# Optimization experiments

Measured on AMD Instinct MI355X. Metric: run time of the kernel, lower is better.

## Reference

```python
import jax, jax.numpy as jnp
import numpy as np
from jax import lax

N = 51200            # total nodes
E = 409600           # edges
FEAT = 768           # BERT emb size
HID = 256            # GGNN out_channels
L = 6                # GGNN layers
NPG = 200            # nodes per graph (conv1d_1 in_channels)
C1_OUT, K1, P1 = 50, 3, 1
C2_OUT, K2 = 20, 1
MP1_K, MP1_S = 3, 2
MP2_K, MP2_S = 2, 2

def _pooled_len(n):
    n = (n - MP1_K) // MP1_S + 1
    n = (n - MP2_K) // MP2_S + 1
    return n

def setup_inputs():
    key = jax.random.key(0)
    ks = jax.random.split(key, 12)
    s = lambda i, shape: jax.random.normal(ks[i], shape, jnp.float32) * 0.02
    fc1_in = C2_OUT * _pooled_len(HID + FEAT)  # 20*255 = 5100
    fc2_in = C2_OUT * _pooled_len(HID)         # 20*63  = 1260
    return dict(
        x=jax.random.normal(ks[0], (N, FEAT), jnp.float32),
        edge_index=jax.random.randint(ks[1], (2, E), 0, N, dtype=jnp.int32),
        W_in=s(2, (HID, FEAT)), b_in=jnp.zeros((HID,), jnp.float32),
        W_ggnn=s(3, (L, HID, HID)),
        W_ih=s(4, (3 * HID, HID)), W_hh=s(5, (3 * HID, HID)),
        b_ih=jnp.zeros((3 * HID,), jnp.float32), b_hh=jnp.zeros((3 * HID,), jnp.float32),
        Wc1=s(6, (C1_OUT, NPG, K1)), bc1=jnp.zeros((C1_OUT,), jnp.float32),
        Wc2=s(7, (C2_OUT, C1_OUT, K2)), bc2=jnp.zeros((C2_OUT,), jnp.float32),
        Wf1=s(8, (1, fc1_in)), bf1=jnp.zeros((1,), jnp.float32),
        Wf2=s(9, (1, fc2_in)), bf2=jnp.zeros((1,), jnp.float32),
    )

def _conv1d(x, w, b, pad):
    y = lax.conv_general_dilated(x, w, (1,), [(pad, pad)], dimension_numbers=('NCH', 'OIH', 'NCH'))
    return y + b[None, :, None]

def _maxpool1d(x, k, s):
    return lax.reduce_window(x, -jnp.inf, lax.max, (1, 1, k), (1, 1, s), 'VALID')

def _ggnn(h0, src, dst, W_ggnn, W_ih, W_hh, b_ih, b_hh):
    h = h0
    for i in range(L):  # fixed small layer loop
        m = h @ W_ggnn[i]                                   # [N, HID]
        agg = jax.ops.segment_sum(m[src], dst, num_segments=N)  # scatter-add aggr
        gi = agg @ W_ih.T + b_ih                            # GRUCell input gates
        gh = h @ W_hh.T + b_hh                              # GRUCell hidden gates
        i_r, i_z, i_n = jnp.split(gi, 3, axis=1)
        h_r, h_z, h_n = jnp.split(gh, 3, axis=1)
        r = jax.nn.sigmoid(i_r + h_r)
        z = jax.nn.sigmoid(i_z + h_z)
        n = jnp.tanh(i_n + r * h_n)
        h = (1.0 - z) * n + z * h
    return h

def _conv_head(h, x, Wc1, bc1, Wc2, bc2, Wf1, bf1, Wf2, bf2):
    concat = jnp.concatenate([h, x], axis=1).reshape(-1, NPG, HID + FEAT)  # [G, NPG, 1024]
    Z = _maxpool1d(jax.nn.relu(_conv1d(concat, Wc1, bc1, P1)), MP1_K, MP1_S)
    Z = _maxpool1d(_conv1d(Z, Wc2, bc2, 0), MP2_K, MP2_S)
    Y = h.reshape(-1, NPG, HID)
    Y = _maxpool1d(jax.nn.relu(_conv1d(Y, Wc1, bc1, P1)), MP1_K, MP1_S)
    Y = _maxpool1d(_conv1d(Y, Wc2, bc2, 0), MP2_K, MP2_S)
    z = Z.reshape(Z.shape[0], -1) @ Wf1.T + bf1
    y = Y.reshape(Y.shape[0], -1) @ Wf2.T + bf2
    # dropout p=0.2 is identity in eval mode
    return jax.nn.sigmoid((z * y).ravel())  # [G]

def reference(x, edge_index, W_in, b_in, W_ggnn, W_ih, W_hh, b_ih, b_hh, Wc1, bc1, Wc2, bc2, Wf1, bf1, Wf2, bf2):
    h0 = x @ W_in.T + b_in
    h = _ggnn(h0, edge_index[0], edge_index[1], W_ggnn, W_ih, W_hh, b_ih, b_hh)
    p = _conv_head(h, x, Wc1, bc1, Wc2, bc2, Wf1, bf1, Wf2, bf2)
    eps = 1e-6
    p = jnp.clip(p, eps, 1.0 - eps)
    z1 = jnp.log(p / (1.0 - p))
    return jnp.stack([jnp.zeros_like(z1), z1], axis=1)  # [G, 2]
```

## Files before the change

kernel.cpp:

```cpp
#include <hip/hip_runtime.h>
#include <math.h>

#define N_NODES 51200
#define N_EDGES 409600
#define FEAT    768
#define HID     256
#define NPG     200
#define G_GRAPHS 256

typedef _Float16 f16x8 __attribute__((ext_vector_type(8)));
typedef _Float16 f16x4 __attribute__((ext_vector_type(4)));
typedef float    f32x4 __attribute__((ext_vector_type(4)));

__device__ __forceinline__ void cvt4(const float* __restrict__ in, _Float16* __restrict__ out, int i) {
    float4 v = *(const float4*)&in[i * 4];
    f16x4 h;
    h[0] = (_Float16)v.x; h[1] = (_Float16)v.y; h[2] = (_Float16)v.z; h[3] = (_Float16)v.w;
    *(f16x4*)&out[i * 4] = h;
}

__global__ __launch_bounds__(256) void k_prep(const float* __restrict__ W_in, const float* __restrict__ W_ih,
                                              const float* __restrict__ W_hh, const float* __restrict__ W_g,
                                              const float* __restrict__ x, const float* __restrict__ Wc1,
                                              const float* __restrict__ bih, const float* __restrict__ bhh,
                                              _Float16* __restrict__ Win_h, _Float16* __restrict__ Wih_h,
                                              _Float16* __restrict__ Whh_h, _Float16* __restrict__ Wg_h,
                                              _Float16* __restrict__ XF, _Float16* __restrict__ Wp,
                                              float* __restrict__ brz, float* __restrict__ bnn,
                                              _Float16* __restrict__ Wrz2,
                                              int* __restrict__ deg, int* __restrict__ fill) {
    int id = blockIdx.x * 256 + threadIdx.x;
    if (id < 49152) { cvt4(W_in, Win_h, id); return; }
    id -= 49152;
    if (id < 49152) { cvt4(W_ih, Wih_h, id); return; }
    id -= 49152;
    if (id < 49152) { cvt4(W_hh, Whh_h, id); return; }
    id -= 49152;
    if (id < 98304) { cvt4(W_g, Wg_h, id); return; }
    id -= 98304;
    if (id < 49152) {
        int ch = id / 12288, r = id - ch * 12288;
        int o = r / 192, k = r - o * 192;
        int dk = k >> 6, cc = k & 63;
        int c = ch * 64 + cc;
        float v = 0.f;
        if (o < 50 && c < NPG) v = Wc1[(o * NPG + c) * 3 + dk];
        Wp[id] = (_Float16)v;
        return;
    }
    id -= 49152;
    if (id < 1024) {
        if (id < 512) brz[id] = bih[id] + bhh[id];
        else {
            int q = id - 512;
            bnn[q] = (q < 256) ? bih[512 + q] : bhh[512 + (q - 256)];
        }
        return;
    }
    id -= 1024;
    if (id < 786432) {
        int l = id >> 17, r = id & 131071;
        int j = r >> 8, c = r & 255;
        Wrz2[(size_t)l * 262144 + j * 512 + 256 + c] = (_Float16)W_hh[j * 256 + c];
        return;
    }
    id -= 786432;
    if (id < 12800) { *(int4*)&deg[id * 4] = make_int4(0, 0, 0, 0); return; }
    id -= 12800;
    if (id < 12800) { *(int4*)&fill[id * 4] = make_int4(0, 0, 0, 0); return; }
    id -= 12800;
    if (id < 9830400) { cvt4(x, XF, id); return; }
}

__global__ __launch_bounds__(256) void k_deg(const int* __restrict__ ei, int* __restrict__ deg) {
    int e = blockIdx.x * 256 + threadIdx.x;
    if (e < N_EDGES) atomicAdd(&deg[ei[N_EDGES + e]], 1);
}

__global__ __launch_bounds__(1024) void k_scan(const int* __restrict__ deg, int* __restrict__ rowp) {
    __shared__ int sums[1024];
    int tid = threadIdx.x;
    int base = tid * 50;
    int s = 0;
    for (int j = 0; j < 50; ++j) s += deg[base + j];
    sums[tid] = s;
    __syncthreads();
    for (int off = 1; off < 1024; off <<= 1) {
        int v = 0;
        if (tid >= off) v = sums[tid - off];
        __syncthreads();
        sums[tid] += v;
        __syncthreads();
    }
    int run = sums[tid] - s;
    for (int j = 0; j < 50; ++j) { rowp[base + j] = run; run += deg[base + j]; }
    if (tid == 1023) rowp[N_NODES] = run;
}

__global__ __launch_bounds__(256) void k_fill(const int* __restrict__ ei, const int* __restrict__ rowp,
                                              int* __restrict__ fill, int* __restrict__ col) {
    int e = blockIdx.x * 256 + threadIdx.x;
    if (e < N_EDGES) {
        int d = ei[N_EDGES + e];
        int pos = atomicAdd(&fill[d], 1);
        col[rowp[d] + pos] = ei[e];
    }
}

template<int AF16, int OUT, int COLB, int SWZ>
__global__ __launch_bounds__(256) void k_gemm2(const void* __restrict__ Av, int lda,
                                               const _Float16* __restrict__ B,
                                               const float* __restrict__ bias,
                                               void* __restrict__ Cv, int ldc,
                                               int K, int wgPerL, int aLStride, int bLStride,
                                               int cLStride, int biasStride) {
    __shared__ _Float16 As[128 * 64];
    __shared__ _Float16 Bs[128 * 64];
    int wg = blockIdx.x;
    int l = wg / wgPerL; wg -= l * wgPerL;
    if (AF16) Av = (const void*)((const _Float16*)Av + (size_t)l * aLStride);
    else      Av = (const void*)((const float*)Av + (size_t)l * aLStride);
    B += (size_t)l * bLStride;
    if (bias) bias += (size_t)l * biasStride;
    if (OUT == 1) Cv = (void*)((_Float16*)Cv + (size_t)l * cLStride);
    else          Cv = (void*)((float*)Cv + (size_t)l * cLStride);
    int rowBase, colBase;
    if (SWZ) {
        int xcd = wg & 7, t = wg >> 3;
        int cb = t % COLB, gidx = t / COLB;
        rowBase = (gidx * 8 + xcd) * 128;
        colBase = cb * 128;
    } else {
        rowBase = (wg / COLB) * 128;
        colBase = (wg % COLB) * 128;
    }
    int tid = threadIdx.x;
    int lane = tid & 63;
    int wid = tid >> 6;
    int wr = wid >> 1, wc = wid & 1;
    f32x4 acc[4][4] = {};
    for (int k0 = 0; k0 < K; k0 += 64) {
        __syncthreads();
        #pragma unroll
        for (int p = 0; p < 4; ++p) {
            int c = p * 256 + tid;
            int row = c >> 3, slot = c & 7;
            int dst = row * 64 + ((slot ^ (row & 7)) * 8);
            if (AF16) {
                const _Float16* srcA = (const _Float16*)Av + (size_t)(rowBase + row) * lda + k0 + slot * 8;
                *(f16x8*)&As[dst] = *(const f16x8*)srcA;
            } else {
                const float* srcA = (const float*)Av + (size_t)(rowBase + row) * lda + k0 + slot * 8;
                float4 f0 = *(const float4*)srcA;
                float4 f1 = *(const float4*)(srcA + 4);
                f16x8 hv;
                hv[0] = (_Float16)f0.x; hv[1] = (_Float16)f0.y; hv[2] = (_Float16)f0.z; hv[3] = (_Float16)f0.w;
                hv[4] = (_Float16)f1.x; hv[5] = (_Float16)f1.y; hv[6] = (_Float16)f1.z; hv[7] = (_Float16)f1.w;
                *(f16x8*)&As[dst] = hv;
            }
            const _Float16* srcB = B + (size_t)(colBase + row) * K + k0 + slot * 8;
            *(f16x8*)&Bs[dst] = *(const f16x8*)srcB;
        }
        __syncthreads();
        #pragma unroll
        for (int ks = 0; ks < 2; ++ks) {
            f16x8 af[4], bf[4];
            #pragma unroll
            for (int mi = 0; mi < 4; ++mi) {
                int row = wr * 64 + mi * 16 + (lane & 15);
                int slot = (lane >> 4) + ks * 4;
                af[mi] = *(const f16x8*)&As[row * 64 + ((slot ^ (row & 7)) * 8)];
            }
            #pragma unroll
            for (int nj = 0; nj < 4; ++nj) {
                int row = wc * 64 + nj * 16 + (lane & 15);
                int slot = (lane >> 4) + ks * 4;
                bf[nj] = *(const f16x8*)&Bs[row * 64 + ((slot ^ (row & 7)) * 8)];
            }
            #pragma unroll
            for (int mi = 0; mi < 4; ++mi)
                #pragma unroll
                for (int nj = 0; nj < 4; ++nj)
                    acc[mi][nj] = __builtin_amdgcn_mfma_f32_16x16x32_f16(af[mi], bf[nj], acc[mi][nj], 0, 0, 0);
        }
    }
    #pragma unroll
    for (int mi = 0; mi < 4; ++mi) {
        #pragma unroll
        for (int nj = 0; nj < 4; ++nj) {
            int col = colBase + wc * 64 + nj * 16 + (lane & 15);
            float bv = bias ? bias[col] : 0.f;
            #pragma unroll
            for (int r = 0; r < 4; ++r) {
                int row = rowBase + wr * 64 + mi * 16 + (lane >> 4) * 4 + r;
                float val = acc[mi][nj][r] + bv;
                if (OUT == 0) ((float*)Cv)[(size_t)row * ldc + col] = val;
                else          ((_Float16*)Cv)[(size_t)row * ldc + col] = (_Float16)val;
            }
        }
    }
}

__global__ __launch_bounds__(256) void k_gemmrz(const _Float16* __restrict__ S, const _Float16* __restrict__ hc,
                                                const _Float16* __restrict__ B, const float* __restrict__ bias,
                                                _Float16* __restrict__ C) {
    __shared__ _Float16 As[128 * 64];
    __shared__ _Float16 Bs[128 * 64];
    int wg = blockIdx.x;
    int xcd = wg & 7, t = wg >> 3;
    int cb = t % 4, gidx = t / 4;
    int rowBase = (gidx * 8 + xcd) * 128;
    int colBase = cb * 128;
    int tid = threadIdx.x;
    int lane = tid & 63;
    int wid = tid >> 6;
    int wr = wid >> 1, wc = wid & 1;
    f32x4 acc[4][4] = {};
    for (int k0 = 0; k0 < 512; k0 += 64) {
        const _Float16* Abase = (k0 < 256) ? S : hc;
        int kk = k0 & 255;
        __syncthreads();
        #pragma unroll
        for (int p = 0; p < 4; ++p) {
            int c = p * 256 + tid;
            int row = c >> 3, slot = c & 7;
            int dst = row * 64 + ((slot ^ (row & 7)) * 8);
            *(f16x8*)&As[dst] = *(const f16x8*)&Abase[(size_t)(rowBase + row) * 256 + kk + slot * 8];
            *(f16x8*)&Bs[dst] = *(const f16x8*)&B[(size_t)(colBase + row) * 512 + k0 + slot * 8];
        }
        __syncthreads();
        #pragma unroll
        for (int ks = 0; ks < 2; ++ks) {
            f16x8 af[4], bf[4];
            #pragma unroll
            for (int mi = 0; mi < 4; ++mi) {
                int row = wr * 64 + mi * 16 + (lane & 15);
                int slot = (lane >> 4) + ks * 4;
                af[mi] = *(const f16x8*)&As[row * 64 + ((slot ^ (row & 7)) * 8)];
            }
            #pragma unroll
            for (int nj = 0; nj < 4; ++nj) {
                int row = wc * 64 + nj * 16 + (lane & 15);
                int slot = (lane >> 4) + ks * 4;
                bf[nj] = *(const f16x8*)&Bs[row * 64 + ((slot ^ (row & 7)) * 8)];
            }
            #pragma unroll
            for (int mi = 0; mi < 4; ++mi)
                #pragma unroll
                for (int nj = 0; nj < 4; ++nj)
                    acc[mi][nj] = __builtin_amdgcn_mfma_f32_16x16x32_f16(af[mi], bf[nj], acc[mi][nj], 0, 0, 0);
        }
    }
    #pragma unroll
    for (int mi = 0; mi < 4; ++mi) {
        #pragma unroll
        for (int nj = 0; nj < 4; ++nj) {
            int col = colBase + wc * 64 + nj * 16 + (lane & 15);
            float bv = bias[col];
            #pragma unroll
            for (int r = 0; r < 4; ++r) {
                int row = rowBase + wr * 64 + mi * 16 + (lane >> 4) * 4 + r;
                C[(size_t)row * 512 + col] = (_Float16)(acc[mi][nj][r] + bv);
            }
        }
    }
}

__global__ __launch_bounds__(512) void k_nngru(const _Float16* __restrict__ S, const _Float16* __restrict__ hc,
                                               const _Float16* __restrict__ B0, const _Float16* __restrict__ B1,
                                               const float* __restrict__ bnn, const _Float16* __restrict__ rz,
                                               _Float16* __restrict__ hn) {
    __shared__ _Float16 As0[128 * 64], As1[128 * 64], Bs0[128 * 64], Bs1[128 * 64];
    int wg = blockIdx.x;
    int xcd = wg & 7, t = wg >> 3;
    int cb = t % 2, gidx = t / 2;
    int rowBase = (gidx * 8 + xcd) * 128;
    int colBase = cb * 128;
    int tid = threadIdx.x;
    int lane = tid & 63;
    int wid = tid >> 6;
    int wr = wid >> 2, wc = wid & 3;
    f32x4 acc0[4][2] = {}, acc1[4][2] = {};
    for (int k0 = 0; k0 < 256; k0 += 64) {
        __syncthreads();
        #pragma unroll
        for (int p = 0; p < 8; ++p) {
            int q = p * 512 + tid;
            int tile = q >> 10;
            int c = q & 1023;
            int row = c >> 3, slot = c & 7;
            int dst = row * 64 + ((slot ^ (row & 7)) * 8);
            const _Float16* src;
            _Float16* d;
            if (tile == 0)      { src = S  + (size_t)(rowBase + row) * 256 + k0 + slot * 8; d = As0; }
            else if (tile == 1) { src = hc + (size_t)(rowBase + row) * 256 + k0 + slot * 8; d = As1; }
            else if (tile == 2) { src = B0 + (size_t)(colBase + row) * 256 + k0 + slot * 8; d = Bs0; }
            else                { src = B1 + (size_t)(colBase + row) * 256 + k0 + slot * 8; d = Bs1; }
            *(f16x8*)&d[dst] = *(const f16x8*)src;
        }
        __syncthreads();
        #pragma unroll
        for (int ks = 0; ks < 2; ++ks) {
            f16x8 a0[4], a1[4], b0[2], b1[2];
            #pragma unroll
            for (int mi = 0; mi < 4; ++mi) {
                int row = wr * 64 + mi * 16 + (lane & 15);
                int slot = (lane >> 4) + ks * 4;
                int off = row * 64 + ((slot ^ (row & 7)) * 8);
                a0[mi] = *(const f16x8*)&As0[off];
                a1[mi] = *(const f16x8*)&As1[off];
            }
            #pragma unroll
            for (int nj = 0; nj < 2; ++nj) {
                int row = wc * 32 + nj * 16 + (lane & 15);
                int slot = (lane >> 4) + ks * 4;
                int off = row * 64 + ((slot ^ (row & 7)) * 8);
                b0[nj] = *(const f16x8*)&Bs0[off];
                b1[nj] = *(const f16x8*)&Bs1[off];
            }
            #pragma unroll
            for (int mi = 0; mi < 4; ++mi)
                #pragma unroll
                for (int nj = 0; nj < 2; ++nj) {
                    acc0[mi][nj] = __builtin_amdgcn_mfma_f32_16x16x32_f16(a0[mi], b0[nj], acc0[mi][nj], 0, 0, 0);
                    acc1[mi][nj] = __builtin_amdgcn_mfma_f32_16x16x32_f16(a1[mi], b1[nj], acc1[mi][nj], 0, 0, 0);
                }
        }
    }
    #pragma unroll
    for (int mi = 0; mi < 4; ++mi) {
        #pragma unroll
        for (int nj = 0; nj < 2; ++nj) {
            int col = colBase + wc * 32 + nj * 16 + (lane & 15);
            float bi = bnn[col], bh = bnn[256 + col];
            #pragma unroll
            for (int r = 0; r < 4; ++r) {
                int row = rowBase + wr * 64 + mi * 16 + (lane >> 4) * 4 + r;
                float rv = (float)rz[(size_t)row * 512 + col];
                float zv = (float)rz[(size_t)row * 512 + 256 + col];
                float rg = 1.f / (1.f + expf(-rv));
                float zg = 1.f / (1.f + expf(-zv));
                float ng = tanhf((acc0[mi][nj][r] + bi) + rg * (acc1[mi][nj][r] + bh));
                float ho = (float)hc[(size_t)row * 256 + col];
                hn[(size_t)row * 256 + col] = (_Float16)((1.f - zg) * ng + zg * ho);
            }
        }
    }
}

__global__ __launch_bounds__(256) void k_agg4(const int* __restrict__ rowp, const int* __restrict__ col,
                                              const _Float16* __restrict__ hc, _Float16* __restrict__ S) {
    int v = blockIdx.x * 4 + (threadIdx.x >> 6);
    int lane = threadIdx.x & 63;
    int beg = rowp[v], end = rowp[v + 1];
    const _Float16* hf = hc + lane * 4;
    float a0 = 0.f, a1 = 0.f, a2 = 0.f, a3 = 0.f;
    int i = beg;
    for (; i + 3 < end; i += 4) {
        int c0 = col[i], c1 = col[i + 1], c2 = col[i + 2], c3 = col[i + 3];
        f16x4 u0 = *(const f16x4*)&hf[(size_t)c0 * 256];
        f16x4 u1 = *(const f16x4*)&hf[(size_t)c1 * 256];
        f16x4 u2 = *(const f16x4*)&hf[(size_t)c2 * 256];
        f16x4 u3 = *(const f16x4*)&hf[(size_t)c3 * 256];
        a0 += ((float)u0[0] + (float)u1[0]) + ((float)u2[0] + (float)u3[0]);
        a1 += ((float)u0[1] + (float)u1[1]) + ((float)u2[1] + (float)u3[1]);
        a2 += ((float)u0[2] + (float)u1[2]) + ((float)u2[2] + (float)u3[2]);
        a3 += ((float)u0[3] + (float)u1[3]) + ((float)u2[3] + (float)u3[3]);
    }
    for (; i < end; ++i) {
        f16x4 u = *(const f16x4*)&hf[(size_t)col[i] * 256];
        a0 += (float)u[0]; a1 += (float)u[1]; a2 += (float)u[2]; a3 += (float)u[3];
    }
    f16x4 o;
    o[0] = (_Float16)a0; o[1] = (_Float16)a1; o[2] = (_Float16)a2; o[3] = (_Float16)a3;
    *(f16x4*)&S[(size_t)v * 256 + lane * 4] = o;
}

__global__ __launch_bounds__(256, 2) void k_conv1m(const _Float16* __restrict__ hf, const _Float16* __restrict__ xf,
                                                   const _Float16* __restrict__ Wp, const float* __restrict__ bc1,
                                                   float* __restrict__ outZ, float* __restrict__ outY) {
    __shared__ _Float16 XT[272 * 64];
    __shared__ _Float16 WL[64 * 192];
    int b = blockIdx.x;
    int g, t0, H;
    float* out;
    if (b < 1024) { g = b >> 2; t0 = (b & 3) * 256; H = 1024; out = outZ; }
    else          { g = b - 1024; t0 = 0; H = 256; out = outY; }
    int tid = threadIdx.x;
    int lane = tid & 63;
    int wn = (tid >> 6) * 64;
    f32x4 acc[4][4] = {};
    for (int ch = 0; ch < 4; ++ch) {
        __syncthreads();
        #pragma unroll
        for (int i = 0; i < 6; ++i) {
            int q = i * 256 + tid;
            int o = q / 24, sk = q - o * 24;
            int skp = (sk & 0x18) | ((sk & 7) ^ (o & 7));
            *(f16x8*)&WL[o * 192 + skp * 8] = *(const f16x8*)&Wp[ch * 12288 + o * 192 + sk * 8];
        }
        for (int u = tid; u < 272; u += 256) {
            int r8 = u / 34, pc = u - r8 * 34;
            int gstart = t0 - 8 + pc * 8;
            int c0 = r8 * 8;
            f16x8 zv;
            #pragma unroll
            for (int q = 0; q < 8; ++q) zv[q] = (_Float16)0.f;
            f16x8 rows[8];
            if (gstart < 0 || gstart >= H) {
                #pragma unroll
                for (int j = 0; j < 8; ++j) rows[j] = zv;
            } else {
                const _Float16* base;
                int stride;
                if (gstart < HID) { base = hf + gstart; stride = 256; }
                else              { base = xf + (gstart - HID); stride = 768; }
                int node0 = g * NPG + ch * 64 + c0;
                #pragma unroll
                for (int j = 0; j < 8; ++j) {
                    int cg = ch * 64 + c0 + j;
                    rows[j] = (cg < NPG) ? *(const f16x8*)&base[(size_t)(node0 + j) * stride] : zv;
                }
            }
            #pragma unroll
            for (int jj = 0; jj < 8; ++jj) {
                f16x8 w;
                #pragma unroll
                for (int j = 0; j < 8; ++j) w[j] = rows[j][jj];
                int p = pc * 8 + jj;
                int slot = r8 ^ jj ^ (pc & 7);
                *(f16x8*)&XT[p * 64 + slot * 8] = w;
            }
        }
        __syncthreads();
        #pragma unroll
        for (int ks = 0; ks < 6; ++ks) {
            int dk = ks >> 1, cs0 = (ks & 1) << 2;
            f16x8 af[4], bf[4];
            #pragma unroll
            for (int mi = 0; mi < 4; ++mi) {
                int o = mi * 16 + (lane & 15);
                int sk = ks * 4 + (lane >> 4);
                int skp = (sk & 0x18) | ((sk & 7) ^ (o & 7));
                af[mi] = *(const f16x8*)&WL[o * 192 + skp * 8];
            }
            #pragma unroll
            for (int nj = 0; nj < 4; ++nj) {
                int tw = wn + nj * 16 + (lane & 15) + dk + 7;
                int sp = (cs0 + (lane >> 4)) ^ (tw & 7) ^ ((tw >> 3) & 7);
                bf[nj] = *(const f16x8*)&XT[tw * 64 + sp * 8];
            }
            #pragma unroll
            for (int mi = 0; mi < 4; ++mi)
                #pragma unroll
                for (int nj = 0; nj < 4; ++nj)
                    acc[mi][nj] = __builtin_amdgcn_mfma_f32_16x16x32_f16(af[mi], bf[nj], acc[mi][nj], 0, 0, 0);
        }
    }
    #pragma unroll
    for (int mi = 0; mi < 4; ++mi) {
        #pragma unroll
        for (int r = 0; r < 4; ++r) {
            int o = mi * 16 + (lane >> 4) * 4 + r;
            if (o < 50) {
                float bv = bc1[o];
                #pragma unroll
                for (int nj = 0; nj < 4; ++nj) {
                    int t = t0 + wn + nj * 16 + (lane & 15);
                    float v = acc[mi][nj][r] + bv;
                    out[(size_t)g * 50 * H + (size_t)o * H + t] = v > 0.f ? v : 0.f;
                }
            }
        }
    }
}

__global__ __launch_bounds__(256) void k_pool1(const float* __restrict__ C1Z, const float* __restrict__ C1Y,
                                               float* __restrict__ P1Z, float* __restrict__ P1Y) {
    int b = blockIdx.x;
    const float* in;
    float* out;
    int H, U, go;
    if (b < 12800) { in = C1Z; out = P1Z; H = 1024; U = 511; go = b; }
    else           { in = C1Y; out = P1Y; H = 256;  U = 127; go = b - 12800; }
    const float* p = in + (size_t)go * H;
    float* q = out + (size_t)go * U;
    for (int u = threadIdx.x; u < U; u += 256) {
        float a = p[2 * u], bb = p[2 * u + 1], c = p[2 * u + 2];
        float mm = a > bb ? a : bb;
        q[u] = mm > c ? mm : c;
    }
}

__global__ __launch_bounds__(256) void k_c2p2(const float* __restrict__ P1Z, const float* __restrict__ P1Y,
                                              const float* __restrict__ Wc2, const float* __restrict__ bc2,
                                              float* __restrict__ P2Z, float* __restrict__ P2Y) {
    int g = blockIdx.x, oy = blockIdx.y;
    const float* P1;
    float* out;
    int U, U2, o2;
    if (oy < 20) { P1 = P1Z; out = P2Z; U = 511; U2 = 255; o2 = oy; }
    else         { P1 = P1Y; out = P2Y; U = 127; U2 = 63;  o2 = oy - 20; }
    float b = bc2[o2];
    for (int u2 = threadIdx.x; u2 < U2; u2 += 256) {
        float a0 = b, a1 = b;
        #pragma unroll 5
        for (int i = 0; i < 50; ++i) {
            float wv = Wc2[o2 * 50 + i];
            const float* p = P1 + ((size_t)g * 50 + i) * U + 2 * u2;
            a0 = fmaf(p[0], wv, a0);
            a1 = fmaf(p[1], wv, a1);
        }
        out[((size_t)g * 20 + o2) * U2 + u2] = a0 > a1 ? a0 : a1;
    }
}

__global__ __launch_bounds__(256) void k_fc(const float* __restrict__ P2Z, const float* __restrict__ P2Y,
                                            const float* __restrict__ Wf1, const float* __restrict__ bf1,
                                            const float* __restrict__ Wf2, const float* __restrict__ bf2,
                                            float* __restrict__ zb, float* __restrict__ yb) {
    __shared__ float red[256];
    int b = blockIdx.x, tid = threadIdx.x;
    int g = b & 255;
    const float* P2;
    const float* Wf;
    const float* bf;
    float* out;
    int len;
    if (b < 256) { P2 = P2Z; Wf = Wf1; bf = bf1; out = zb; len = 20 * 255; }
    else         { P2 = P2Y; Wf = Wf2; bf = bf2; out = yb; len = 20 * 63; }
    const float* p = P2 + (size_t)g * len;
    float s = 0.f;
    for (int i = tid; i < len; i += 256) s = fmaf(p[i], Wf[i], s);
    red[tid] = s;
    __syncthreads();
    for (int off = 128; off > 0; off >>= 1) {
        if (tid < off) red[tid] += red[tid + off];
        __syncthreads();
    }
    if (tid == 0) out[g] = red[0] + bf[0];
}

__global__ __launch_bounds__(256) void k_final(const float* __restrict__ z, const float* __restrict__ y,
                                               float* __restrict__ out) {
    int g = threadIdx.x;
    float t = z[g] * y[g];
    float p = 1.f / (1.f + expf(-t));
    p = fminf(fmaxf(p, 1e-6f), 1.f - 1e-6f);
    float z1 = logf(p / (1.f - p));
    out[2 * g] = 0.f;
    out[2 * g + 1] = z1;
}

extern "C" void kernel_launch(void* const* d_in, const int* in_sizes, int n_in,
                              void* d_out, int out_size, void* d_ws, size_t ws_size,
                              hipStream_t stream) {
    const float* x     = (const float*)d_in[0];
    const int*   ei    = (const int*)d_in[1];
    const float* W_in  = (const float*)d_in[2];
    const float* b_in  = (const float*)d_in[3];
    const float* W_g   = (const float*)d_in[4];
    const float* W_ih  = (const float*)d_in[5];
    const float* W_hh  = (const float*)d_in[6];
    const float* b_ih  = (const float*)d_in[7];
    const float* b_hh  = (const float*)d_in[8];
    const float* Wc1   = (const float*)d_in[9];
    const float* bc1   = (const float*)d_in[10];
    const float* Wc2   = (const float*)d_in[11];
    const float* bc2   = (const float*)d_in[12];
    const float* Wf1   = (const float*)d_in[13];
    const float* bf1   = (const float*)d_in[14];
    const float* Wf2   = (const float*)d_in[15];
    const float* bf2   = (const float*)d_in[16];

    float* ws = (float*)d_ws;
    const size_t OFF_S   = 0;
    const size_t OFF_HA  = 6553600;
    const size_t OFF_HB  = 13107200;
    const size_t OFF_RZ  = 19660800;
    const size_t OFF_XF  = 32768000;
    const size_t OFF_WF  = 52428800;
    const size_t OFF_BRZ = 53927936;
    const size_t OFF_BNN = 53928448;
    const size_t OFF_INT = 53928960;
    const size_t OFF_ZB  = 54492200;
    const size_t OFF_P2Z = 54500000;
    const size_t OFF_P2Y = 55900000;

    _Float16* S  = (_Float16*)(ws + OFF_S);
    _Float16* HA = (_Float16*)(ws + OFF_HA);
    _Float16* HB = (_Float16*)(ws + OFF_HB);
    _Float16* RZ = (_Float16*)(ws + OFF_RZ);
    _Float16* XF = (_Float16*)(ws + OFF_XF);

    _Float16* Win_h = (_Float16*)(ws + OFF_WF);
    _Float16* Wih_h = Win_h + 196608;
    _Float16* Whh_h = Wih_h + 196608;
    _Float16* Wg_h  = Whh_h + 196608;
    _Float16* Wrz2  = Wg_h  + 393216;
    _Float16* Wni2  = Wrz2  + 1572864;
    _Float16* Wp    = Wni2  + 393216;
    _Float16* Whhn  = Whh_h + 512 * 256;
    float* brz = ws + OFF_BRZ;
    float* bnn = ws + OFF_BNN;

    int* deg  = (int*)(ws + OFF_INT);
    int* fill = deg + N_NODES;
    int* rowp = fill + N_NODES;
    int* col  = rowp + (N_NODES + 1);
    float* zb = ws + OFF_ZB;
    float* yb = zb + 256;

    float* C1Z = ws + OFF_RZ;
    float* P1Z = ws + OFF_HB;
    float* C1Y = ws + OFF_S;
    float* P1Y = ws + 3300000;
    float* P2Z = ws + OFF_P2Z;
    float* P2Y = ws + OFF_P2Y;

    k_prep<<<42728, 256, 0, stream>>>(W_in, W_ih, W_hh, W_g, x, Wc1, b_ih, b_hh,
                                      Win_h, Wih_h, Whh_h, Wg_h, XF, Wp, brz, bnn, Wrz2,
                                      deg, fill);
    k_gemm2<1, 1, 2, 0><<<48, 256, 0, stream>>>(Wih_h, 256, Wg_h, nullptr,
                                                Wrz2, 512, 256, 8, 0, 65536, 262144, 0);
    k_gemm2<1, 1, 2, 0><<<24, 256, 0, stream>>>(Wih_h + 512 * 256, 256, Wg_h, nullptr,
                                                Wni2, 256, 256, 4, 0, 65536, 65536, 0);

    k_deg<<<N_EDGES / 256, 256, 0, stream>>>(ei, deg);
    k_scan<<<1, 1024, 0, stream>>>(deg, rowp);
    k_fill<<<N_EDGES / 256, 256, 0, stream>>>(ei, rowp, fill, col);

    k_gemm2<1, 1, 2, 1><<<800, 256, 0, stream>>>(XF, FEAT, Win_h, b_in, HA, HID,
                                                 FEAT, 800, 0, 0, 0, 0);

    for (int l = 0; l < 6; ++l) {
        _Float16* hc = (l & 1) ? HB : HA;
        _Float16* hn = (l & 1) ? HA : HB;
        k_agg4<<<12800, 256, 0, stream>>>(rowp, col, hc, S);
        k_gemmrz<<<1600, 256, 0, stream>>>(S, hc, Wrz2 + (size_t)l * 262144, brz, RZ);
        k_nngru<<<800, 512, 0, stream>>>(S, hc, Wni2 + (size_t)l * 65536, Whhn, bnn, RZ, hn);
    }

    k_conv1m<<<1280, 256, 0, stream>>>(HA, XF, Wp, bc1, C1Z, C1Y);
    k_pool1<<<25600, 256, 0, stream>>>(C1Z, C1Y, P1Z, P1Y);
    k_c2p2<<<dim3(G_GRAPHS, 40), 256, 0, stream>>>(P1Z, P1Y, Wc2, bc2, P2Z, P2Y);
    k_fc<<<512, 256, 0, stream>>>(P2Z, P2Y, Wf1, bf1, Wf2, bf2, zb, yb);

    k_final<<<1, 256, 0, stream>>>(zb, yb, (float*)d_out);
}
```

Measured before the change: 1.124 ms.

## Fuse r/z gate GEMM into GRU n-gate kernel, drop RZ intermediate buffer

Merges the separate r/z gate GEMM kernel into the n-gate GRU kernel. Each block first computes the r and z pre-activations for its 128x128 output tile (K=512 over [S,hc]), applies the sigmoids in registers, then runs the n-gate GEMMs and the GRU update. This removes the RZ write and readback to global memory and one launch per layer. In exchange it holds more accumulators per thread, which raises register pressure under launch_bounds(512,2).

```diff
diff --git a/kernel.cpp b/kernel.cpp
--- a/kernel.cpp
+++ b/kernel.cpp
@@ -201,76 +201,11 @@
     }
 }
 
-__global__ __launch_bounds__(256) void k_gemmrz(const _Float16* __restrict__ S, const _Float16* __restrict__ hc,
-                                                const _Float16* __restrict__ B, const float* __restrict__ bias,
-                                                _Float16* __restrict__ C) {
-    __shared__ _Float16 As[128 * 64];
-    __shared__ _Float16 Bs[128 * 64];
-    int wg = blockIdx.x;
-    int xcd = wg & 7, t = wg >> 3;
-    int cb = t % 4, gidx = t / 4;
-    int rowBase = (gidx * 8 + xcd) * 128;
-    int colBase = cb * 128;
-    int tid = threadIdx.x;
-    int lane = tid & 63;
-    int wid = tid >> 6;
-    int wr = wid >> 1, wc = wid & 1;
-    f32x4 acc[4][4] = {};
-    for (int k0 = 0; k0 < 512; k0 += 64) {
-        const _Float16* Abase = (k0 < 256) ? S : hc;
-        int kk = k0 & 255;
-        __syncthreads();
-        #pragma unroll
-        for (int p = 0; p < 4; ++p) {
-            int c = p * 256 + tid;
-            int row = c >> 3, slot = c & 7;
-            int dst = row * 64 + ((slot ^ (row & 7)) * 8);
-            *(f16x8*)&As[dst] = *(const f16x8*)&Abase[(size_t)(rowBase + row) * 256 + kk + slot * 8];
-            *(f16x8*)&Bs[dst] = *(const f16x8*)&B[(size_t)(colBase + row) * 512 + k0 + slot * 8];
-        }
-        __syncthreads();
-        #pragma unroll
-        for (int ks = 0; ks < 2; ++ks) {
-            f16x8 af[4], bf[4];
-            #pragma unroll
-            for (int mi = 0; mi < 4; ++mi) {
-                int row = wr * 64 + mi * 16 + (lane & 15);
-                int slot = (lane >> 4) + ks * 4;
-                af[mi] = *(const f16x8*)&As[row * 64 + ((slot ^ (row & 7)) * 8)];
-            }
-            #pragma unroll
-            for (int nj = 0; nj < 4; ++nj) {
-                int row = wc * 64 + nj * 16 + (lane & 15);
-                int slot = (lane >> 4) + ks * 4;
-                bf[nj] = *(const f16x8*)&Bs[row * 64 + ((slot ^ (row & 7)) * 8)];
-            }
-            #pragma unroll
-            for (int mi = 0; mi < 4; ++mi)
-                #pragma unroll
-                for (int nj = 0; nj < 4; ++nj)
-                    acc[mi][nj] = __builtin_amdgcn_mfma_f32_16x16x32_f16(af[mi], bf[nj], acc[mi][nj], 0, 0, 0);
-        }
-    }
-    #pragma unroll
-    for (int mi = 0; mi < 4; ++mi) {
-        #pragma unroll
-        for (int nj = 0; nj < 4; ++nj) {
-            int col = colBase + wc * 64 + nj * 16 + (lane & 15);
-            float bv = bias[col];
-            #pragma unroll
-            for (int r = 0; r < 4; ++r) {
-                int row = rowBase + wr * 64 + mi * 16 + (lane >> 4) * 4 + r;
-                C[(size_t)row * 512 + col] = (_Float16)(acc[mi][nj][r] + bv);
-            }
-        }
-    }
-}
-
-__global__ __launch_bounds__(512) void k_nngru(const _Float16* __restrict__ S, const _Float16* __restrict__ hc,
-                                               const _Float16* __restrict__ B0, const _Float16* __restrict__ B1,
-                                               const float* __restrict__ bnn, const _Float16* __restrict__ rz,
-                                               _Float16* __restrict__ hn) {
-    __shared__ _Float16 As0[128 * 64], As1[128 * 64], Bs0[128 * 64], Bs1[128 * 64];
+__global__ __launch_bounds__(512, 2) void k_rzng(const _Float16* __restrict__ S, const _Float16* __restrict__ hc,
+                                                 const _Float16* __restrict__ Wrz, const float* __restrict__ brz,
+                                                 const _Float16* __restrict__ B0, const _Float16* __restrict__ B1,
+                                                 const float* __restrict__ bnn, _Float16* __restrict__ hn) {
+    __shared__ _Float16 T0[128 * 64], T1[128 * 64], T2[128 * 64], T3[128 * 64];
     int wg = blockIdx.x;
     int xcd = wg & 7, t = wg >> 3;
     int cb = t % 2, gidx = t / 2;
@@ -280,6 +215,62 @@
     int lane = tid & 63;
     int wid = tid >> 6;
     int wr = wid >> 2, wc = wid & 3;
+    f32x4 accr[4][2] = {}, accz[4][2] = {};
+    for (int k0 = 0; k0 < 512; k0 += 64) {
+        const _Float16* Ab = (k0 < 256) ? S : hc;
+        int kk = k0 & 255;
+        __syncthreads();
+        #pragma unroll
+        for (int p = 0; p < 6; ++p) {
+            int q = p * 512 + tid;
+            int tile = q >> 10;
+            int c = q & 1023;
+            int row = c >> 3, slot = c & 7;
+            int dst = row * 64 + ((slot ^ (row & 7)) * 8);
+            if (tile == 0)      *(f16x8*)&T0[dst] = *(const f16x8*)&Ab[(size_t)(rowBase + row) * 256 + kk + slot * 8];
+            else if (tile == 1) *(f16x8*)&T1[dst] = *(const f16x8*)&Wrz[(size_t)(colBase + row) * 512 + k0 + slot * 8];
+            else                *(f16x8*)&T2[dst] = *(const f16x8*)&Wrz[(size_t)(256 + colBase + row) * 512 + k0 + slot * 8];
+        }
+        __syncthreads();
+        #pragma unroll
+        for (int ks = 0; ks < 2; ++ks) {
+            f16x8 af[4], br[2], bz[2];
+            #pragma unroll
+            for (int mi = 0; mi < 4; ++mi) {
+                int row = wr * 64 + mi * 16 + (lane & 15);
+                int slot = (lane >> 4) + ks * 4;
+                af[mi] = *(const f16x8*)&T0[row * 64 + ((slot ^ (row & 7)) * 8)];
+            }
+            #pragma unroll
+            for (int nj = 0; nj < 2; ++nj) {
+                int row = wc * 32 + nj * 16 + (lane & 15);
+                int slot = (lane >> 4) + ks * 4;
+                int off = row * 64 + ((slot ^ (row & 7)) * 8);
+                br[nj] = *(const f16x8*)&T1[off];
+                bz[nj] = *(const f16x8*)&T2[off];
+            }
+            #pragma unroll
+            for (int mi = 0; mi < 4; ++mi)
+                #pragma unroll
+                for (int nj = 0; nj < 2; ++nj) {
+                    accr[mi][nj] = __builtin_amdgcn_mfma_f32_16x16x32_f16(af[mi], br[nj], accr[mi][nj], 0, 0, 0);
+                    accz[mi][nj] = __builtin_amdgcn_mfma_f32_16x16x32_f16(af[mi], bz[nj], accz[mi][nj], 0, 0, 0);
+                }
+        }
+    }
+    f32x4 rg[4][2], zg[4][2];
+    #pragma unroll
+    for (int mi = 0; mi < 4; ++mi)
+        #pragma unroll
+        for (int nj = 0; nj < 2; ++nj) {
+            int col = colBase + wc * 32 + nj * 16 + (lane & 15);
+            float br_ = brz[col], bz_ = brz[256 + col];
+            #pragma unroll
+            for (int r = 0; r < 4; ++r) {
+                rg[mi][nj][r] = 1.f / (1.f + expf(-(accr[mi][nj][r] + br_)));
+                zg[mi][nj][r] = 1.f / (1.f + expf(-(accz[mi][nj][r] + bz_)));
+            }
+        }
     f32x4 acc0[4][2] = {}, acc1[4][2] = {};
     for (int k0 = 0; k0 < 256; k0 += 64) {
         __syncthreads();
@@ -292,10 +283,10 @@
             int dst = row * 64 + ((slot ^ (row & 7)) * 8);
             const _Float16* src;
             _Float16* d;
-            if (tile == 0)      { src = S  + (size_t)(rowBase + row) * 256 + k0 + slot * 8; d = As0; }
-            else if (tile == 1) { src = hc + (size_t)(rowBase + row) * 256 + k0 + slot * 8; d = As1; }
-            else if (tile == 2) { src = B0 + (size_t)(colBase + row) * 256 + k0 + slot * 8; d = Bs0; }
-            else                { src = B1 + (size_t)(colBase + row) * 256 + k0 + slot * 8; d = Bs1; }
+            if (tile == 0)      { src = S  + (size_t)(rowBase + row) * 256 + k0 + slot * 8; d = T0; }
+            else if (tile == 1) { src = hc + (size_t)(rowBase + row) * 256 + k0 + slot * 8; d = T1; }
+            else if (tile == 2) { src = B0 + (size_t)(colBase + row) * 256 + k0 + slot * 8; d = T2; }
+            else                { src = B1 + (size_t)(colBase + row) * 256 + k0 + slot * 8; d = T3; }
             *(f16x8*)&d[dst] = *(const f16x8*)src;
         }
         __syncthreads();
@@ -307,16 +298,16 @@
                 int row = wr * 64 + mi * 16 + (lane & 15);
                 int slot = (lane >> 4) + ks * 4;
                 int off = row * 64 + ((slot ^ (row & 7)) * 8);
-                a0[mi] = *(const f16x8*)&As0[off];
-                a1[mi] = *(const f16x8*)&As1[off];
+                a0[mi] = *(const f16x8*)&T0[off];
+                a1[mi] = *(const f16x8*)&T1[off];
             }
             #pragma unroll
             for (int nj = 0; nj < 2; ++nj) {
                 int row = wc * 32 + nj * 16 + (lane & 15);
                 int slot = (lane >> 4) + ks * 4;
                 int off = row * 64 + ((slot ^ (row & 7)) * 8);
-                b0[nj] = *(const f16x8*)&Bs0[off];
-                b1[nj] = *(const f16x8*)&Bs1[off];
+                b0[nj] = *(const f16x8*)&T2[off];
+                b1[nj] = *(const f16x8*)&T3[off];
             }
             #pragma unroll
             for (int mi = 0; mi < 4; ++mi)
@@ -336,13 +327,9 @@
             #pragma unroll
             for (int r = 0; r < 4; ++r) {
                 int row = rowBase + wr * 64 + mi * 16 + (lane >> 4) * 4 + r;
-                float rv = (float)rz[(size_t)row * 512 + col];
-                float zv = (float)rz[(size_t)row * 512 + 256 + col];
-                float rg = 1.f / (1.f + expf(-rv));
-                float zg = 1.f / (1.f + expf(-zv));
-                float ng = tanhf((acc0[mi][nj][r] + bi) + rg * (acc1[mi][nj][r] + bh));
+                float ng = tanhf((acc0[mi][nj][r] + bi) + rg[mi][nj][r] * (acc1[mi][nj][r] + bh));
                 float ho = (float)hc[(size_t)row * 256 + col];
-                hn[(size_t)row * 256 + col] = (_Float16)((1.f - zg) * ng + zg * ho);
+                hn[(size_t)row * 256 + col] = (_Float16)((1.f - zg[mi][nj][r]) * ng + zg[mi][nj][r] * ho);
             }
         }
     }
@@ -590,7 +577,6 @@
     _Float16* S  = (_Float16*)(ws + OFF_S);
     _Float16* HA = (_Float16*)(ws + OFF_HA);
     _Float16* HB = (_Float16*)(ws + OFF_HB);
-    _Float16* RZ = (_Float16*)(ws + OFF_RZ);
     _Float16* XF = (_Float16*)(ws + OFF_XF);
 
     _Float16* Win_h = (_Float16*)(ws + OFF_WF);
@@ -637,8 +623,8 @@
         _Float16* hc = (l & 1) ? HB : HA;
         _Float16* hn = (l & 1) ? HA : HB;
         k_agg4<<<12800, 256, 0, stream>>>(rowp, col, hc, S);
-        k_gemmrz<<<1600, 256, 0, stream>>>(S, hc, Wrz2 + (size_t)l * 262144, brz, RZ);
-        k_nngru<<<800, 512, 0, stream>>>(S, hc, Wni2 + (size_t)l * 65536, Whhn, bnn, RZ, hn);
+        k_rzng<<<800, 512, 0, stream>>>(S, hc, Wrz2 + (size_t)l * 262144, brz,
+                                        Wni2 + (size_t)l * 65536, Whhn, bnn, hn);
     }
 
     k_conv1m<<<1280, 256, 0, stream>>>(HA, XF, Wp, bc1, C1Z, C1Y);
```

Measured after the change: 1.253 ms. +11.5%, slower.
